# Performance work log

Hardware: AMD Instinct MI355X
Metric: run time of the kernel (lower is better)

The kernel has to match this reference:

```python
import math
import jax, jax.numpy as jnp
import numpy as np

DIM = 256
HEADS = 4
TAU = 1e-3
TOPK = 64


def setup_inputs() -> dict:
    key = jax.random.key(0)
    ks = jax.random.split(key, 11)
    B, N, D = 4, 1024, DIM
    s = 1.0 / math.sqrt(D)
    return {
        "F_cls": jax.random.normal(ks[0], (B, N, D), jnp.float32),
        "F_seg": jax.random.normal(ks[1], (B, N, D), jnp.float32),
        "F_age": jax.random.normal(ks[2], (B, N, D), jnp.float32),
        "Wq": jax.random.normal(ks[3], (D, D), jnp.float32) * s,
        "bq": jnp.zeros((D,), jnp.float32),
        "Wk": jax.random.normal(ks[4], (D, D), jnp.float32) * s,
        "bk": jnp.zeros((D,), jnp.float32),
        "Wv": jax.random.normal(ks[5], (D, D), jnp.float32) * s,
        "bv": jnp.zeros((D,), jnp.float32),
        "Wo": jax.random.normal(ks[6], (D, D), jnp.float32) * s,
        "bo": jnp.zeros((D,), jnp.float32),
    }


def reference(F_cls, F_seg, F_age, Wq, bq, Wk, bk, Wv, bv, Wo, bo):
    # Concatenate the three task branches along tokens: (B, 3N, D)
    X = jnp.concatenate([F_cls, F_seg, F_age], axis=1)
    # L1 soft-thresholding
    Xs = jnp.sign(X) * jnp.maximum(jnp.abs(X) - TAU, 0.0)
    B, TN, D = Xs.shape
    N = F_cls.shape[1]
    H, Dh = HEADS, D // HEADS
    # per-sample channel saliency and top-k channel mask
    sal = jnp.abs(Xs).mean(axis=1)                      # (B, D)
    _, idx = jax.lax.top_k(sal, TOPK)                   # (B, k)
    mask = jnp.zeros((B, D), bool).at[jnp.arange(B)[:, None], idx].set(True)
    Xt = Xs * mask[:, None, :]                          # (B, TN, D)
    # shared K/V over all tokens; Q over all tokens equals the concat of the
    # three per-branch q_proj outputs (same weights), so one fused attention
    # is mathematically identical to the three original calls.
    Q = Xt @ Wq.T + bq
    K = Xt @ Wk.T + bk
    V = Xt @ Wv.T + bv
    def heads(x):
        return x.reshape(B, TN, H, Dh).transpose(0, 2, 1, 3)  # (B,H,TN,Dh)
    Qh, Kh, Vh = heads(Q), heads(K), heads(V)
    logits = jnp.einsum("bhqd,bhkd->bhqk", Qh, Kh) / math.sqrt(Dh)
    A = jax.nn.softmax(logits, axis=-1)
    out = jnp.einsum("bhqk,bhkd->bhqd", A, Vh)
    out = out.transpose(0, 2, 1, 3).reshape(B, TN, D)
    out = out @ Wo.T + bo
    return (out[:, 0:N], out[:, N:2 * N], out[:, 2 * N:3 * N])
```

## Files before the change

### kernel.cpp

```cpp
#include <hip/hip_runtime.h>
#include <math.h>

typedef __attribute__((ext_vector_type(8))) short bf16x8;
typedef __attribute__((ext_vector_type(16))) float f32x16;

#define Bsz 4
#define Nn 1024
#define TN 3072
#define Dd 256
#define Hh 4
#define DH 64
#define TAUc 1e-3f
#define QSCALE 0.1803368801111f

#define SALP_OFF 0
#define IDX_OFF  98304
#define XCB_OFF  98560
#define WCT_OFF  491776
#define QB_OFF   590080
#define KB_OFF   2162944
#define VT_OFF   3735808
#define OP0_OFF  5308672
#define OP1_OFF  8454400
#define SML_OFF  11600128

__device__ __forceinline__ ushort f2b(float f) {
    uint u = __float_as_uint(f);
    u += 0x7fffu + ((u >> 16) & 1u);
    return (ushort)(u >> 16);
}
__device__ __forceinline__ uint pk2(float a, float b) {
    return (uint)f2b(a) | ((uint)f2b(b) << 16);
}
__device__ __forceinline__ uint trunc_pk(float a, float b) {
    return (__float_as_uint(a) >> 16) | (__float_as_uint(b) & 0xFFFF0000u);
}
__device__ __forceinline__ float hi_f(float a) {
    return __uint_as_float(__float_as_uint(a) & 0xFFFF0000u);
}
__device__ __forceinline__ uint cvtpk(float a, float b) {
    uint r;
    asm("v_cvt_pk_bf16_f32 %0, %1, %2" : "=v"(r) : "v"(a), "v"(b));
    return r;
}
__device__ __forceinline__ float ex2(float x) {
    return __builtin_amdgcn_exp2f(x);
}
__device__ __forceinline__ void gld16(const ushort* g, ushort* l) {
    __builtin_amdgcn_global_load_lds(
        (const __attribute__((address_space(1))) uint*)g,
        (__attribute__((address_space(3))) uint*)l, 16, 0, 0);
}
union U4B8 { uint u[4]; bf16x8 v; };
__device__ __forceinline__ bf16x8 ld8(const ushort* p) { return *(const bf16x8*)p; }

__global__ __launch_bounds__(256) void k_sal(
        const float* __restrict__ F0, const float* __restrict__ F1,
        const float* __restrict__ F2, float* __restrict__ salp) {
    int b = blockIdx.x / 96;
    int slab = blockIdx.x - b * 96;
    int t0 = slab * 32;
    int seg = t0 >> 10, tt0 = t0 & 1023;
    const float* F = (seg == 0) ? F0 : (seg == 1 ? F1 : F2);
    const float* base = &F[(size_t)((b << 10) + tt0) * Dd + threadIdx.x];
    float acc = 0.f;
    #pragma unroll 4
    for (int r = 0; r < 32; ++r) {
        float x = base[(size_t)r * Dd];
        acc += fmaxf(fabsf(x) - TAUc, 0.f);
    }
    salp[blockIdx.x * 256 + threadIdx.x] = acc;
}

__global__ void k_topk(const float* __restrict__ salp, int* __restrict__ idx) {
    __shared__ float v[256];
    __shared__ int cnt;
    int b = blockIdx.x, tid = threadIdx.x;
    float myval = 0.f;
    const float* p = &salp[(size_t)b * 96 * 256 + tid];
    #pragma unroll 4
    for (int s = 0; s < 96; ++s) myval += p[s * 256];
    v[tid] = myval;
    if (tid == 0) cnt = 0;
    __syncthreads();
    for (int k = 2; k <= 256; k <<= 1)
        for (int j = k >> 1; j > 0; j >>= 1) {
            int ixj = tid ^ j;
            if (ixj > tid) {
                float a = v[tid], c = v[ixj];
                bool up = ((tid & k) == 0);
                if ((a > c) == up) { v[tid] = c; v[ixj] = a; }
            }
            __syncthreads();
        }
    float thr = v[192];
    if (myval >= thr) {
        int p2 = atomicAdd(&cnt, 1);
        if (p2 < 64) idx[b * 64 + p2] = tid;
    }
}

__global__ __launch_bounds__(256) void k_gather(
        const float* __restrict__ F0, const float* __restrict__ F1,
        const float* __restrict__ F2,
        const float* __restrict__ Wq, const float* __restrict__ Wk,
        const float* __restrict__ Wv, const int* __restrict__ idx,
        uint* __restrict__ Xcb, uint* __restrict__ Wct) {
    __shared__ float xs[32 * 260];
    __shared__ int ids[64];
    int tid = threadIdx.x;
    if (blockIdx.x < 384) {
        int b = blockIdx.x / 96;
        int t0 = (blockIdx.x - b * 96) * 32;
        if (tid < 64) ids[tid] = idx[b * 64 + tid];
        int seg = t0 >> 10, tt0 = t0 & 1023;
        const float* F = (seg == 0) ? F0 : (seg == 1 ? F1 : F2);
        const float* base = &F[(size_t)((b << 10) + tt0) * Dd];
        #pragma unroll
        for (int i = 0; i < 8; ++i) {
            int i0 = tid + i * 256;
            int r = i0 >> 6, c4 = (i0 & 63) << 2;
            float4 x = *(const float4*)&base[(size_t)r * Dd + c4];
            x.x = copysignf(fmaxf(fabsf(x.x) - TAUc, 0.f), x.x);
            x.y = copysignf(fmaxf(fabsf(x.y) - TAUc, 0.f), x.y);
            x.z = copysignf(fmaxf(fabsf(x.z) - TAUc, 0.f), x.z);
            x.w = copysignf(fmaxf(fabsf(x.w) - TAUc, 0.f), x.w);
            *(float4*)&xs[r * 260 + c4] = x;
        }
        __syncthreads();
        #pragma unroll
        for (int i = 0; i < 4; ++i) {
            int i0 = tid + i * 256;
            int r = i0 >> 5, jp = i0 & 31;
            float x0 = xs[r * 260 + ids[2 * jp]];
            float x1 = xs[r * 260 + ids[2 * jp + 1]];
            Xcb[(size_t)(b * TN + t0 + r) * 32 + jp] = pk2(x0, x1);
        }
    } else {
        int gid = (blockIdx.x - 384) * 256 + tid;
        int b = gid / 24576;
        if (tid < 64) ids[tid] = idx[b * 64 + tid];
        __syncthreads();
        int rem = gid - b * 24576;
        int mat = rem / 8192;
        int rem2 = rem - mat * 8192;
        int dout = rem2 >> 5, jp = rem2 & 31;
        const float* Wm = (mat == 0) ? Wq : (mat == 1 ? Wk : Wv);
        float w0 = Wm[(size_t)dout * 256 + ids[2 * jp]];
        float w1 = Wm[(size_t)dout * 256 + ids[2 * jp + 1]];
        Wct[((size_t)(b * 3 + mat) * 256 + dout) * 32 + jp] = pk2(w0, w1);
    }
}

__global__ __launch_bounds__(256) void k_qkv(
        const ushort* __restrict__ Xcb, const ushort* __restrict__ Wct,
        const float* __restrict__ bq, const float* __restrict__ bk,
        const float* __restrict__ bv,
        ushort* __restrict__ Qh, ushort* __restrict__ Kh, ushort* __restrict__ Vt) {
    int wave = threadIdx.x >> 6, lane = threadIdx.x & 63;
    int l31 = lane & 31, h = lane >> 5;
    int W = blockIdx.x * 4 + wave;
    int b = W / 576;
    int r = W - b * 576;
    int mat = r / 192;
    int p = r - mat * 192;
    const ushort* Xb = Xcb + (size_t)b * TN * 64;
    const ushort* Wm = Wct + (size_t)(b * 3 + mat) * 256 * 64;
    f32x16 c[4];
    #pragma unroll
    for (int nt = 0; nt < 4; ++nt)
        #pragma unroll
        for (int q = 0; q < 16; ++q) c[nt][q] = 0.f;
    if (mat < 2) {
        int mtt = p % 96, ng = p / 96;
        const ushort* arow = &Xb[(size_t)(mtt * 32 + l31) * 64];
        #pragma unroll
        for (int kc = 0; kc < 4; ++kc) {
            bf16x8 af = ld8(arow + kc * 16 + 8 * h);
            #pragma unroll
            for (int nt = 0; nt < 4; ++nt) {
                bf16x8 bf = ld8(&Wm[(size_t)(ng * 128 + nt * 32 + l31) * 64 + kc * 16 + 8 * h]);
                c[nt] = __builtin_amdgcn_mfma_f32_32x32x16_bf16(af, bf, c[nt], 0, 0, 0);
            }
        }
        if (mat == 0) {
            #pragma unroll
            for (int nt = 0; nt < 4; ++nt) {
                int dout = ng * 128 + nt * 32 + l31;
                int head = dout >> 6, d63 = dout & 63;
                float bb = bq[dout];
                size_t obase = ((size_t)(b * 4 + head) * TN + mtt * 32) * 64 + d63;
                #pragma unroll
                for (int u = 0; u < 16; ++u) {
                    int trow = (u & 3) + 8 * (u >> 2) + 4 * h;
                    Qh[obase + (size_t)trow * 64] = f2b((c[nt][u] + bb) * QSCALE);
                }
            }
        } else {
            #pragma unroll
            for (int nt = 0; nt < 4; ++nt) {
                int dout = ng * 128 + nt * 32 + l31;
                int head = dout >> 6, d63 = dout & 63;
                float bb = bk[dout];
                size_t base = (size_t)(b * 4 + head) * 196608;
                #pragma unroll
                for (int u = 0; u < 16; ++u) {
                    int trow = (u & 3) + 8 * (u >> 2) + 4 * h;
                    int t = mtt * 32 + trow;
                    int row = t & 127, tile = t >> 7;
                    int fk = (row ^ (row >> 3)) & 7;
                    Kh[base + (size_t)tile * 8192 + row * 64 +
                       (((d63 >> 3) ^ fk) << 3) + (d63 & 7)] = f2b(c[nt][u] + bb);
                }
            }
        }
    } else {
        int mtv = p & 7, tg = p >> 3;
        const ushort* arow = &Wm[(size_t)(mtv * 32 + l31) * 64];
        #pragma unroll
        for (int kc = 0; kc < 4; ++kc) {
            bf16x8 af = ld8(arow + kc * 16 + 8 * h);
            #pragma unroll
            for (int nt = 0; nt < 4; ++nt) {
                bf16x8 bf = ld8(&Xb[(size_t)(tg * 128 + nt * 32 + l31) * 64 + kc * 16 + 8 * h]);
                c[nt] = __builtin_amdgcn_mfma_f32_32x32x16_bf16(af, bf, c[nt], 0, 0, 0);
            }
        }
        int head = mtv >> 1;
        int sl = (l31 & 19) | ((l31 & 4) << 1) | ((l31 & 8) >> 1);
        size_t vbase = (size_t)(b * 4 + head) * 196608 + (size_t)tg * 8192;
        #pragma unroll
        for (int nt = 0; nt < 4; ++nt) {
            int cc = (nt * 32 + sl) >> 3;
            int elem = sl & 7;
            #pragma unroll
            for (int u = 0; u < 16; ++u) {
                int dout = mtv * 32 + (u & 3) + 8 * (u >> 2) + 4 * h;
                int row = dout & 63;
                int fv = (row ^ (row >> 3)) & 7;
                int ch = (cc & 8) | ((cc & 7) ^ fv);
                Vt[vbase + row * 128 + ch * 8 + elem] = f2b(c[nt][u] + bv[dout]);
            }
        }
    }
}

__global__ __launch_bounds__(256, 3) void k_attn(
        const ushort* __restrict__ Qg, const ushort* __restrict__ Kg,
        const ushort* __restrict__ Vtg,
        float* __restrict__ OP0, float* __restrict__ OP1,
        float* __restrict__ Sml) {
    __shared__ __align__(16) ushort Ks[2][64 * 64];
    __shared__ __align__(16) ushort Vts[2][64 * 64];
    int bid = blockIdx.x;
    int xcd = bid & 7, j0 = bid >> 3;
    int bh = xcd * 2 + (j0 / 48);
    int rem = j0 % 48;
    int qt = rem >> 1, ksplit = rem & 1;
    int b = bh >> 2, hh = bh & 3;
    int tid = threadIdx.x, wave = tid >> 6, lane = tid & 63;
    int l31 = lane & 31, h = lane >> 5;
    int q0 = qt * 128 + wave * 32;
    const ushort* Qb = Qg + ((size_t)bh * TN + q0 + l31) * DH;
    bf16x8 qf[4];
    #pragma unroll
    for (int kc = 0; kc < 4; ++kc) qf[kc] = ld8(&Qb[kc * 16 + 8 * h]);

    const ushort* Ktb = Kg + (size_t)bh * 196608 + (size_t)ksplit * 98304;
    const ushort* Vtb = Vtg + (size_t)bh * 196608 + (size_t)ksplit * 98304;

    int koff0 = tid * 8, koff1 = tid * 8 + 2048;
    int voff0 = (tid >> 3) * 128 + (tid & 7) * 8;
    int voff1 = voff0 + 4096;

    f32x16 o0, o1;
    #pragma unroll
    for (int q = 0; q < 16; ++q) { o0[q] = 0.f; o1[q] = 0.f; }
    f32x16 zf;
    #pragma unroll
    for (int q = 0; q < 16; ++q) zf[q] = 0.f;
    float lrun = 0.f;

    int fq0 = (l31 ^ (l31 >> 3)) & 7;
    int fq1 = ((32 + l31) ^ ((32 + l31) >> 3)) & 7;
    int r0c = l31 * 64, r1c = (32 + l31) * 64;

    auto stage = [&](int ht, ushort* KsD, ushort* VtsD) {
        const ushort* ksrc = Ktb + (size_t)ht * 4096;
        const ushort* vsrc = Vtb + (size_t)((ht >> 1) * 8192 + (ht & 1) * 64);
        gld16(ksrc + koff0, KsD + koff0);
        gld16(ksrc + koff1, KsD + koff1);
        gld16(vsrc + voff0, VtsD + koff0);
        gld16(vsrc + voff1, VtsD + koff1);
    };

    auto compute = [&](const ushort* KsB, const ushort* VtsB) {
        f32x16 s0, s1;
        __builtin_amdgcn_s_setprio(1);
        {
            bf16x8 k0 = ld8(&KsB[r0c + ((h ^ fq0) << 3)]);
            s0 = __builtin_amdgcn_mfma_f32_32x32x16_bf16(k0, qf[0], zf, 0, 0, 0);
        }
        #pragma unroll
        for (int kc = 1; kc < 4; ++kc) {
            bf16x8 k0 = ld8(&KsB[r0c + (((2 * kc + h) ^ fq0) << 3)]);
            s0 = __builtin_amdgcn_mfma_f32_32x32x16_bf16(k0, qf[kc], s0, 0, 0, 0);
        }
        {
            bf16x8 k1 = ld8(&KsB[r1c + ((h ^ fq1) << 3)]);
            s1 = __builtin_amdgcn_mfma_f32_32x32x16_bf16(k1, qf[0], zf, 0, 0, 0);
        }
        #pragma unroll
        for (int kc = 1; kc < 4; ++kc) {
            bf16x8 k1 = ld8(&KsB[r1c + (((2 * kc + h) ^ fq1) << 3)]);
            s1 = __builtin_amdgcn_mfma_f32_32x32x16_bf16(k1, qf[kc], s1, 0, 0, 0);
        }
        __builtin_amdgcn_s_setprio(0);
        U4B8 pk4[4];
        float ps0 = 0.f, ps1 = 0.f, ps2 = 0.f, ps3 = 0.f;
        #pragma unroll
        for (int u = 0; u < 8; ++u) {
            float pa = ex2(s0[2 * u]), pb = ex2(s0[2 * u + 1]);
            ps0 += pa; ps1 += pb;
            pk4[u >> 2].u[u & 3] = cvtpk(pa, pb);
        }
        __builtin_amdgcn_s_setprio(1);
        #pragma unroll
        for (int kc2 = 0; kc2 < 2; ++kc2) {
            int ch = 2 * kc2 + h;
            bf16x8 v0f = ld8(&VtsB[r0c + ((ch ^ fq0) << 3)]);
            bf16x8 v1f = ld8(&VtsB[r1c + ((ch ^ fq1) << 3)]);
            o0 = __builtin_amdgcn_mfma_f32_32x32x16_bf16(pk4[kc2].v, v0f, o0, 0, 0, 0);
            o1 = __builtin_amdgcn_mfma_f32_32x32x16_bf16(pk4[kc2].v, v1f, o1, 0, 0, 0);
        }
        __builtin_amdgcn_s_setprio(0);
        #pragma unroll
        for (int u = 0; u < 8; ++u) {
            float pa = ex2(s1[2 * u]), pb = ex2(s1[2 * u + 1]);
            ps2 += pa; ps3 += pb;
            pk4[2 + (u >> 2)].u[u & 3] = cvtpk(pa, pb);
        }
        lrun += (ps0 + ps1) + (ps2 + ps3);
        __builtin_amdgcn_s_setprio(1);
        #pragma unroll
        for (int kc2 = 2; kc2 < 4; ++kc2) {
            int ch = 2 * kc2 + h;
            bf16x8 v0f = ld8(&VtsB[r0c + ((ch ^ fq0) << 3)]);
            bf16x8 v1f = ld8(&VtsB[r1c + ((ch ^ fq1) << 3)]);
            o0 = __builtin_amdgcn_mfma_f32_32x32x16_bf16(pk4[kc2].v, v0f, o0, 0, 0, 0);
            o1 = __builtin_amdgcn_mfma_f32_32x32x16_bf16(pk4[kc2].v, v1f, o1, 0, 0, 0);
        }
        __builtin_amdgcn_s_setprio(0);
    };

    stage(0, Ks[0], Vts[0]);
    __syncthreads();
    #pragma unroll 1
    for (int t = 0; t < 24; t += 2) {
        stage(t + 1, Ks[1], Vts[1]);
        compute(Ks[0], Vts[0]);
        __syncthreads();
        if (t + 2 < 24) stage(t + 2, Ks[0], Vts[0]);
        compute(Ks[1], Vts[1]);
        __syncthreads();
    }

    lrun += __shfl_xor(lrun, 32);

    float* OP = ksplit ? OP1 : OP0;
    #pragma unroll
    for (int q = 0; q < 16; ++q) {
        int qrow = (q & 3) + 8 * (q >> 2) + 4 * h;
        int t = q0 + qrow;
        size_t base = ((size_t)b * TN + t) * Dd + hh * 64;
        OP[base + l31] = o0[q];
        OP[base + 32 + l31] = o1[q];
    }
    if (h == 0)
        Sml[(size_t)ksplit * 49152 + (size_t)bh * TN + q0 + l31] = lrun;
}

__global__ __launch_bounds__(256) void k_out(
        const float* __restrict__ OP0, const float* __restrict__ OP1,
        const float* __restrict__ Sml, const float* __restrict__ Wo,
        const float* __restrict__ bo, float* __restrict__ out) {
    __shared__ __align__(16) ushort Ms[2][64][64];
    __shared__ float invsh[64 * 4];
    int nd4 = blockIdx.y;
    int R0 = blockIdx.x * 64;
    int b = R0 / TN;
    int tloc0 = R0 - b * TN;
    int tid = threadIdx.x, wave = tid >> 6, lane = tid & 63;
    int l31 = lane & 31, h = lane >> 5;
    int wt = wave & 1, wd = wave >> 1;
    {
        int hd = tid >> 6, t = tid & 63;
        size_t o = (size_t)(b * 4 + hd) * TN + tloc0 + t;
        invsh[t * 4 + hd] = 1.f / (Sml[o] + Sml[49152 + o]);
    }
    int dout = nd4 * 64 + wd * 32 + l31;
    float bb = bo[dout];
    const float* wrow = &Wo[(size_t)dout * 256];
    int st_t = tid >> 2, st_c = tid & 3;
    int fst = (st_t ^ (st_t >> 3)) & 7;
    size_t gbase = ((size_t)(b * TN + tloc0 + st_t)) * 256 + st_c * 8;
    int trow = wt * 32 + l31;
    int ftr = (trow ^ (trow >> 3)) & 7;
    f32x16 acc;
    #pragma unroll
    for (int q = 0; q < 16; ++q) acc[q] = 0.f;

    auto stage_load = [&](int st, int buf) {
        size_t ob = gbase + (size_t)st * 32;
        float4 x0 = *(const float4*)&OP0[ob];
        float4 x1 = *(const float4*)&OP0[ob + 4];
        float4 y0 = *(const float4*)&OP1[ob];
        float4 y1 = *(const float4*)&OP1[ob + 4];
        float s = invsh[st_t * 4 + (st >> 1)];
        float m0 = (x0.x + y0.x) * s, m1 = (x0.y + y0.y) * s;
        float m2 = (x0.z + y0.z) * s, m3 = (x0.w + y0.w) * s;
        float m4 = (x1.x + y1.x) * s, m5 = (x1.y + y1.y) * s;
        float m6 = (x1.z + y1.z) * s, m7 = (x1.w + y1.w) * s;
        uint4 hi = { trunc_pk(m0, m1), trunc_pk(m2, m3),
                     trunc_pk(m4, m5), trunc_pk(m6, m7) };
        uint4 lo = { trunc_pk(m0 - hi_f(m0), m1 - hi_f(m1)),
                     trunc_pk(m2 - hi_f(m2), m3 - hi_f(m3)),
                     trunc_pk(m4 - hi_f(m4), m5 - hi_f(m5)),
                     trunc_pk(m6 - hi_f(m6), m7 - hi_f(m7)) };
        *(uint4*)&Ms[buf][st_t][(st_c ^ fst) * 8] = hi;
        *(uint4*)&Ms[buf][st_t][((4 + st_c) ^ fst) * 8] = lo;
    };

    __syncthreads();
    stage_load(0, 0);
    #pragma unroll 1
    for (int st = 0; st < 8; ++st) {
        __syncthreads();
        if (st < 7) stage_load(st + 1, (st + 1) & 1);
        int buf = st & 1;
        #pragma unroll
        for (int kc = 0; kc < 2; ++kc) {
            bf16x8 ah = *(const bf16x8*)&Ms[buf][trow][((2 * kc + h) ^ ftr) * 8];
            bf16x8 al = *(const bf16x8*)&Ms[buf][trow][((4 + 2 * kc + h) ^ ftr) * 8];
            int din0 = st * 32 + kc * 16 + 8 * h;
            float4 w0 = *(const float4*)&wrow[din0];
            float4 w1 = *(const float4*)&wrow[din0 + 4];
            U4B8 wh, wl;
            wh.u[0] = trunc_pk(w0.x, w0.y); wh.u[1] = trunc_pk(w0.z, w0.w);
            wh.u[2] = trunc_pk(w1.x, w1.y); wh.u[3] = trunc_pk(w1.z, w1.w);
            wl.u[0] = trunc_pk(w0.x - hi_f(w0.x), w0.y - hi_f(w0.y));
            wl.u[1] = trunc_pk(w0.z - hi_f(w0.z), w0.w - hi_f(w0.w));
            wl.u[2] = trunc_pk(w1.x - hi_f(w1.x), w1.y - hi_f(w1.y));
            wl.u[3] = trunc_pk(w1.z - hi_f(w1.z), w1.w - hi_f(w1.w));
            acc = __builtin_amdgcn_mfma_f32_32x32x16_bf16(ah, wh.v, acc, 0, 0, 0);
            acc = __builtin_amdgcn_mfma_f32_32x32x16_bf16(al, wh.v, acc, 0, 0, 0);
            acc = __builtin_amdgcn_mfma_f32_32x32x16_bf16(ah, wl.v, acc, 0, 0, 0);
        }
    }
    #pragma unroll
    for (int u = 0; u < 16; ++u) {
        int tloc = tloc0 + wt * 32 + (u & 3) + 8 * (u >> 2) + 4 * h;
        int chunk = tloc >> 10, tt = tloc & 1023;
        out[(size_t)chunk * (Bsz * Nn * Dd) + ((size_t)(b * Nn + tt)) * Dd + dout] =
            acc[u] + bb;
    }
}

extern "C" void kernel_launch(void* const* d_in, const int* in_sizes, int n_in,
                              void* d_out, int out_size, void* d_ws, size_t ws_size,
                              hipStream_t stream) {
    const float* F0 = (const float*)d_in[0];
    const float* F1 = (const float*)d_in[1];
    const float* F2 = (const float*)d_in[2];
    const float* Wq = (const float*)d_in[3];
    const float* bq = (const float*)d_in[4];
    const float* Wk = (const float*)d_in[5];
    const float* bk = (const float*)d_in[6];
    const float* Wv = (const float*)d_in[7];
    const float* bv = (const float*)d_in[8];
    const float* Wo = (const float*)d_in[9];
    const float* bo = (const float*)d_in[10];
    float* ws = (float*)d_ws;
    float* out = (float*)d_out;

    int* idxp = (int*)(ws + IDX_OFF);
    uint* Xcb = (uint*)(ws + XCB_OFF);
    uint* Wct = (uint*)(ws + WCT_OFF);
    ushort* Qb16 = (ushort*)(ws + QB_OFF);
    ushort* Kb16 = (ushort*)(ws + KB_OFF);
    ushort* Vt16 = (ushort*)(ws + VT_OFF);
    float* OP0 = ws + OP0_OFF;
    float* OP1 = ws + OP1_OFF;
    float* Sml = ws + SML_OFF;

    k_sal<<<384, 256, 0, stream>>>(F0, F1, F2, ws + SALP_OFF);
    k_topk<<<Bsz, 256, 0, stream>>>(ws + SALP_OFF, idxp);
    k_gather<<<768, 256, 0, stream>>>(F0, F1, F2, Wq, Wk, Wv, idxp, Xcb, Wct);
    k_qkv<<<576, 256, 0, stream>>>((const ushort*)Xcb, (const ushort*)Wct,
                                   bq, bk, bv, Qb16, Kb16, Vt16);
    k_attn<<<768, 256, 0, stream>>>(Qb16, Kb16, Vt16, OP0, OP1, Sml);
    k_out<<<dim3(192, 4), 256, 0, stream>>>(OP0, OP1, Sml, Wo, bo, out);
}
```

Before: 171.4 us.

## Generalize attention key-split to four partitions when workspace allows

Parameterizes the flash-attention key split so k_attn can divide the key sequence into four chunks instead of two. When the workspace is large enough this doubles the grid to 1536 blocks, and k_out sums four partial outputs and denominators. Launch bounds rise to 5 blocks per SM to improve occupancy and latency hiding. The cost is more partial-output memory traffic in k_out and shorter per-block loops with more prologue overhead.

```diff
diff --git a/kernel.cpp b/kernel.cpp
--- a/kernel.cpp
+++ b/kernel.cpp
@@ -21,8 +21,10 @@
 #define KB_OFF   2162944
 #define VT_OFF   3735808
 #define OP0_OFF  5308672
-#define OP1_OFF  8454400
-#define SML_OFF  11600128
+#define OPSTR    3145728
+#define SML2_OFF 11600128
+#define SML4_OFF 17891584
+#define WS4_NEED ((size_t)(17891584 + 4 * 49152) * 4)
 
 __device__ __forceinline__ ushort f2b(float f) {
     uint u = __float_as_uint(f);
@@ -245,18 +247,21 @@
     }
 }
 
-__global__ __launch_bounds__(256, 3) void k_attn(
+__global__ __launch_bounds__(256, 5) void k_attn(
         const ushort* __restrict__ Qg, const ushort* __restrict__ Kg,
         const ushort* __restrict__ Vtg,
-        float* __restrict__ OP0, float* __restrict__ OP1,
-        float* __restrict__ Sml) {
+        float* __restrict__ OPb, float* __restrict__ Sml, int nspl) {
     __shared__ __align__(16) ushort Ks[2][64 * 64];
     __shared__ __align__(16) ushort Vts[2][64 * 64];
     int bid = blockIdx.x;
     int xcd = bid & 7, j0 = bid >> 3;
-    int bh = xcd * 2 + (j0 / 48);
-    int rem = j0 % 48;
-    int qt = rem >> 1, ksplit = rem & 1;
+    int pb = 24 * nspl;
+    int bhl = j0 / pb;
+    int bh = xcd * 2 + bhl;
+    int rem = j0 - bhl * pb;
+    int qt = rem / nspl;
+    int ks = rem - qt * nspl;
+    int nhalf = 48 / nspl;
     int b = bh >> 2, hh = bh & 3;
     int tid = threadIdx.x, wave = tid >> 6, lane = tid & 63;
     int l31 = lane & 31, h = lane >> 5;
@@ -266,8 +271,8 @@
     #pragma unroll
     for (int kc = 0; kc < 4; ++kc) qf[kc] = ld8(&Qb[kc * 16 + 8 * h]);
 
-    const ushort* Ktb = Kg + (size_t)bh * 196608 + (size_t)ksplit * 98304;
-    const ushort* Vtb = Vtg + (size_t)bh * 196608 + (size_t)ksplit * 98304;
+    const ushort* Ktb = Kg + (size_t)bh * 196608 + (size_t)ks * (nhalf * 4096);
+    const ushort* Vtb = Vtg + (size_t)bh * 196608 + (size_t)ks * (nhalf * 4096);
 
     int koff0 = tid * 8, koff1 = tid * 8 + 2048;
     int voff0 = (tid >> 3) * 128 + (tid & 7) * 8;
@@ -320,9 +325,9 @@
         float ps0 = 0.f, ps1 = 0.f, ps2 = 0.f, ps3 = 0.f;
         #pragma unroll
         for (int u = 0; u < 8; ++u) {
-            float pa = ex2(s0[2 * u]), pb = ex2(s0[2 * u + 1]);
-            ps0 += pa; ps1 += pb;
-            pk4[u >> 2].u[u & 3] = cvtpk(pa, pb);
+            float pa = ex2(s0[2 * u]), pb2 = ex2(s0[2 * u + 1]);
+            ps0 += pa; ps1 += pb2;
+            pk4[u >> 2].u[u & 3] = cvtpk(pa, pb2);
         }
         __builtin_amdgcn_s_setprio(1);
         #pragma unroll
@@ -336,9 +341,9 @@
         __builtin_amdgcn_s_setprio(0);
         #pragma unroll
         for (int u = 0; u < 8; ++u) {
-            float pa = ex2(s1[2 * u]), pb = ex2(s1[2 * u + 1]);
-            ps2 += pa; ps3 += pb;
-            pk4[2 + (u >> 2)].u[u & 3] = cvtpk(pa, pb);
+            float pa = ex2(s1[2 * u]), pb2 = ex2(s1[2 * u + 1]);
+            ps2 += pa; ps3 += pb2;
+            pk4[2 + (u >> 2)].u[u & 3] = cvtpk(pa, pb2);
         }
         lrun += (ps0 + ps1) + (ps2 + ps3);
         __builtin_amdgcn_s_setprio(1);
@@ -356,18 +361,18 @@
     stage(0, Ks[0], Vts[0]);
     __syncthreads();
     #pragma unroll 1
-    for (int t = 0; t < 24; t += 2) {
+    for (int t = 0; t < nhalf; t += 2) {
         stage(t + 1, Ks[1], Vts[1]);
         compute(Ks[0], Vts[0]);
         __syncthreads();
-        if (t + 2 < 24) stage(t + 2, Ks[0], Vts[0]);
+        if (t + 2 < nhalf) stage(t + 2, Ks[0], Vts[0]);
         compute(Ks[1], Vts[1]);
         __syncthreads();
     }
 
     lrun += __shfl_xor(lrun, 32);
 
-    float* OP = ksplit ? OP1 : OP0;
+    float* OP = OPb + (size_t)ks * OPSTR;
     #pragma unroll
     for (int q = 0; q < 16; ++q) {
         int qrow = (q & 3) + 8 * (q >> 2) + 4 * h;
@@ -377,13 +382,13 @@
         OP[base + 32 + l31] = o1[q];
     }
     if (h == 0)
-        Sml[(size_t)ksplit * 49152 + (size_t)bh * TN + q0 + l31] = lrun;
+        Sml[(size_t)ks * 49152 + (size_t)bh * TN + q0 + l31] = lrun;
 }
 
 __global__ __launch_bounds__(256) void k_out(
-        const float* __restrict__ OP0, const float* __restrict__ OP1,
-        const float* __restrict__ Sml, const float* __restrict__ Wo,
-        const float* __restrict__ bo, float* __restrict__ out) {
+        const float* __restrict__ OPb, const float* __restrict__ Sml,
+        const float* __restrict__ Wo, const float* __restrict__ bo,
+        float* __restrict__ out, int nspl) {
     __shared__ __align__(16) ushort Ms[2][64][64];
     __shared__ float invsh[64 * 4];
     int nd4 = blockIdx.y;
@@ -396,7 +401,10 @@
     {
         int hd = tid >> 6, t = tid & 63;
         size_t o = (size_t)(b * 4 + hd) * TN + tloc0 + t;
-        invsh[t * 4 + hd] = 1.f / (Sml[o] + Sml[49152 + o]);
+        float ssum = 0.f;
+        #pragma unroll 2
+        for (int sp = 0; sp < nspl; ++sp) ssum += Sml[(size_t)sp * 49152 + o];
+        invsh[t * 4 + hd] = 1.f / ssum;
     }
     int dout = nd4 * 64 + wd * 32 + l31;
     float bb = bo[dout];
@@ -412,15 +420,19 @@
 
     auto stage_load = [&](int st, int buf) {
         size_t ob = gbase + (size_t)st * 32;
-        float4 x0 = *(const float4*)&OP0[ob];
-        float4 x1 = *(const float4*)&OP0[ob + 4];
-        float4 y0 = *(const float4*)&OP1[ob];
-        float4 y1 = *(const float4*)&OP1[ob + 4];
+        float a0 = 0.f, a1 = 0.f, a2 = 0.f, a3 = 0.f;
+        float a4 = 0.f, a5 = 0.f, a6 = 0.f, a7 = 0.f;
+        #pragma unroll 2
+        for (int sp = 0; sp < nspl; ++sp) {
+            const float* P = OPb + (size_t)sp * OPSTR;
+            float4 u0 = *(const float4*)&P[ob];
+            float4 u1 = *(const float4*)&P[ob + 4];
+            a0 += u0.x; a1 += u0.y; a2 += u0.z; a3 += u0.w;
+            a4 += u1.x; a5 += u1.y; a6 += u1.z; a7 += u1.w;
+        }
         float s = invsh[st_t * 4 + (st >> 1)];
-        float m0 = (x0.x + y0.x) * s, m1 = (x0.y + y0.y) * s;
-        float m2 = (x0.z + y0.z) * s, m3 = (x0.w + y0.w) * s;
-        float m4 = (x1.x + y1.x) * s, m5 = (x1.y + y1.y) * s;
-        float m6 = (x1.z + y1.z) * s, m7 = (x1.w + y1.w) * s;
+        float m0 = a0 * s, m1 = a1 * s, m2 = a2 * s, m3 = a3 * s;
+        float m4 = a4 * s, m5 = a5 * s, m6 = a6 * s, m7 = a7 * s;
         uint4 hi = { trunc_pk(m0, m1), trunc_pk(m2, m3),
                      trunc_pk(m4, m5), trunc_pk(m6, m7) };
         uint4 lo = { trunc_pk(m0 - hi_f(m0), m1 - hi_f(m1)),
@@ -490,14 +502,15 @@
     ushort* Kb16 = (ushort*)(ws + KB_OFF);
     ushort* Vt16 = (ushort*)(ws + VT_OFF);
     float* OP0 = ws + OP0_OFF;
-    float* OP1 = ws + OP1_OFF;
-    float* Sml = ws + SML_OFF;
+
+    int nspl = (ws_size >= WS4_NEED) ? 4 : 2;
+    float* Sml = (nspl == 4) ? (ws + SML4_OFF) : (ws + SML2_OFF);
 
     k_sal<<<384, 256, 0, stream>>>(F0, F1, F2, ws + SALP_OFF);
     k_topk<<<Bsz, 256, 0, stream>>>(ws + SALP_OFF, idxp);
     k_gather<<<768, 256, 0, stream>>>(F0, F1, F2, Wq, Wk, Wv, idxp, Xcb, Wct);
     k_qkv<<<576, 256, 0, stream>>>((const ushort*)Xcb, (const ushort*)Wct,
                                    bq, bk, bv, Qb16, Kb16, Vt16);
-    k_attn<<<768, 256, 0, stream>>>(Qb16, Kb16, Vt16, OP0, OP1, Sml);
-    k_out<<<dim3(192, 4), 256, 0, stream>>>(OP0, OP1, Sml, Wo, bo, out);
-}
+    k_attn<<<384 * nspl, 256, 0, stream>>>(Qb16, Kb16, Vt16, OP0, Sml, nspl);
+    k_out<<<dim3(192, 4), 256, 0, stream>>>(OP0, Sml, Wo, bo, out, nspl);
+}
```

Result: slower. 438.9 us (+156.0%).

## Pre-split Wo into bf16 hi/lo once and use shuffle-based bitonic top-k

Applied to the files above, without the earlier changes.

Adds 64 extra blocks to the gather kernel that convert Wo once into packed bf16 hi and lo halves in workspace. k_out then loads those ready-made operands instead of re-splitting fp32 weights in every block and k-step, which halves the weight bytes read and removes the per-step conversion ALU work. Separately, the top-k bitonic sort keeps values in registers and uses wave shuffles for strides below 64, so it only goes through shared memory and barriers for the larger strides. Costs are a little more workspace and a slightly longer gather launch.

```diff
diff --git a/kernel.cpp b/kernel.cpp
--- a/kernel.cpp
+++ b/kernel.cpp
@@ -23,6 +23,7 @@
 #define OP0_OFF  5308672
 #define OP1_OFF  8454400
 #define SML_OFF  11600128
+#define WOP_OFF  11698432
 
 __device__ __forceinline__ ushort f2b(float f) {
     uint u = __float_as_uint(f);
@@ -73,27 +74,35 @@
 }
 
 __global__ void k_topk(const float* __restrict__ salp, int* __restrict__ idx) {
-    __shared__ float v[256];
+    __shared__ float xw[256];
+    __shared__ float thrs;
     __shared__ int cnt;
     int b = blockIdx.x, tid = threadIdx.x;
     float myval = 0.f;
     const float* p = &salp[(size_t)b * 96 * 256 + tid];
     #pragma unroll 4
     for (int s = 0; s < 96; ++s) myval += p[s * 256];
-    v[tid] = myval;
     if (tid == 0) cnt = 0;
+    float v = myval;
+    for (int k = 2; k <= 256; k <<= 1) {
+        for (int j = k >> 1; j > 0; j >>= 1) {
+            bool up = ((tid & k) == 0);
+            float ov;
+            if (j >= 64) {
+                xw[tid] = v;
+                __syncthreads();
+                ov = xw[tid ^ j];
+                __syncthreads();
+            } else {
+                ov = __shfl_xor(v, j);
+            }
+            bool lowhalf = ((tid & j) == 0);
+            v = (lowhalf == up) ? fminf(v, ov) : fmaxf(v, ov);
+        }
+    }
+    if (tid == 192) thrs = v;
     __syncthreads();
-    for (int k = 2; k <= 256; k <<= 1)
-        for (int j = k >> 1; j > 0; j >>= 1) {
-            int ixj = tid ^ j;
-            if (ixj > tid) {
-                float a = v[tid], c = v[ixj];
-                bool up = ((tid & k) == 0);
-                if ((a > c) == up) { v[tid] = c; v[ixj] = a; }
-            }
-            __syncthreads();
-        }
-    float thr = v[192];
+    float thr = thrs;
     if (myval >= thr) {
         int p2 = atomicAdd(&cnt, 1);
         if (p2 < 64) idx[b * 64 + p2] = tid;
@@ -104,8 +113,10 @@
         const float* __restrict__ F0, const float* __restrict__ F1,
         const float* __restrict__ F2,
         const float* __restrict__ Wq, const float* __restrict__ Wk,
-        const float* __restrict__ Wv, const int* __restrict__ idx,
-        uint* __restrict__ Xcb, uint* __restrict__ Wct) {
+        const float* __restrict__ Wv, const float* __restrict__ Wo,
+        const int* __restrict__ idx,
+        uint* __restrict__ Xcb, uint* __restrict__ Wct,
+        uint* __restrict__ Wop) {
     __shared__ float xs[32 * 260];
     __shared__ int ids[64];
     int tid = threadIdx.x;
@@ -136,7 +147,7 @@
             float x1 = xs[r * 260 + ids[2 * jp + 1]];
             Xcb[(size_t)(b * TN + t0 + r) * 32 + jp] = pk2(x0, x1);
         }
-    } else {
+    } else if (blockIdx.x < 768) {
         int gid = (blockIdx.x - 384) * 256 + tid;
         int b = gid / 24576;
         if (tid < 64) ids[tid] = idx[b * 64 + tid];
@@ -149,6 +160,15 @@
         float w0 = Wm[(size_t)dout * 256 + ids[2 * jp]];
         float w1 = Wm[(size_t)dout * 256 + ids[2 * jp + 1]];
         Wct[((size_t)(b * 3 + mat) * 256 + dout) * 32 + jp] = pk2(w0, w1);
+    } else {
+        int gid2 = (blockIdx.x - 768) * 256 + tid;
+        int dout = gid2 >> 6, g = gid2 & 63;
+        float4 w = *(const float4*)&Wo[(size_t)dout * 256 + g * 4];
+        uint* row = &Wop[(size_t)dout * 256];
+        row[g * 2]       = trunc_pk(w.x, w.y);
+        row[g * 2 + 1]   = trunc_pk(w.z, w.w);
+        row[128 + g * 2] = trunc_pk(w.x - hi_f(w.x), w.y - hi_f(w.y));
+        row[128 + g * 2 + 1] = trunc_pk(w.z - hi_f(w.z), w.w - hi_f(w.w));
     }
 }
 
@@ -382,7 +402,7 @@
 
 __global__ __launch_bounds__(256) void k_out(
         const float* __restrict__ OP0, const float* __restrict__ OP1,
-        const float* __restrict__ Sml, const float* __restrict__ Wo,
+        const float* __restrict__ Sml, const uint* __restrict__ Wop,
         const float* __restrict__ bo, float* __restrict__ out) {
     __shared__ __align__(16) ushort Ms[2][64][64];
     __shared__ float invsh[64 * 4];
@@ -400,7 +420,7 @@
     }
     int dout = nd4 * 64 + wd * 32 + l31;
     float bb = bo[dout];
-    const float* wrow = &Wo[(size_t)dout * 256];
+    const uint* wrow = &Wop[(size_t)dout * 256];
     int st_t = tid >> 2, st_c = tid & 3;
     int fst = (st_t ^ (st_t >> 3)) & 7;
     size_t gbase = ((size_t)(b * TN + tloc0 + st_t)) * 256 + st_c * 8;
@@ -443,18 +463,11 @@
             bf16x8 ah = *(const bf16x8*)&Ms[buf][trow][((2 * kc + h) ^ ftr) * 8];
             bf16x8 al = *(const bf16x8*)&Ms[buf][trow][((4 + 2 * kc + h) ^ ftr) * 8];
             int din0 = st * 32 + kc * 16 + 8 * h;
-            float4 w0 = *(const float4*)&wrow[din0];
-            float4 w1 = *(const float4*)&wrow[din0 + 4];
-            U4B8 wh, wl;
-            wh.u[0] = trunc_pk(w0.x, w0.y); wh.u[1] = trunc_pk(w0.z, w0.w);
-            wh.u[2] = trunc_pk(w1.x, w1.y); wh.u[3] = trunc_pk(w1.z, w1.w);
-            wl.u[0] = trunc_pk(w0.x - hi_f(w0.x), w0.y - hi_f(w0.y));
-            wl.u[1] = trunc_pk(w0.z - hi_f(w0.z), w0.w - hi_f(w0.w));
-            wl.u[2] = trunc_pk(w1.x - hi_f(w1.x), w1.y - hi_f(w1.y));
-            wl.u[3] = trunc_pk(w1.z - hi_f(w1.z), w1.w - hi_f(w1.w));
-            acc = __builtin_amdgcn_mfma_f32_32x32x16_bf16(ah, wh.v, acc, 0, 0, 0);
-            acc = __builtin_amdgcn_mfma_f32_32x32x16_bf16(al, wh.v, acc, 0, 0, 0);
-            acc = __builtin_amdgcn_mfma_f32_32x32x16_bf16(ah, wl.v, acc, 0, 0, 0);
+            bf16x8 whv = *(const bf16x8*)&wrow[din0 >> 1];
+            bf16x8 wlv = *(const bf16x8*)&wrow[128 + (din0 >> 1)];
+            acc = __builtin_amdgcn_mfma_f32_32x32x16_bf16(ah, whv, acc, 0, 0, 0);
+            acc = __builtin_amdgcn_mfma_f32_32x32x16_bf16(al, whv, acc, 0, 0, 0);
+            acc = __builtin_amdgcn_mfma_f32_32x32x16_bf16(ah, wlv, acc, 0, 0, 0);
         }
     }
     #pragma unroll
@@ -492,12 +505,14 @@
     float* OP0 = ws + OP0_OFF;
     float* OP1 = ws + OP1_OFF;
     float* Sml = ws + SML_OFF;
+    uint* Wop = (uint*)(ws + WOP_OFF);
 
     k_sal<<<384, 256, 0, stream>>>(F0, F1, F2, ws + SALP_OFF);
     k_topk<<<Bsz, 256, 0, stream>>>(ws + SALP_OFF, idxp);
-    k_gather<<<768, 256, 0, stream>>>(F0, F1, F2, Wq, Wk, Wv, idxp, Xcb, Wct);
+    k_gather<<<832, 256, 0, stream>>>(F0, F1, F2, Wq, Wk, Wv, Wo, idxp,
+                                      Xcb, Wct, Wop);
     k_qkv<<<576, 256, 0, stream>>>((const ushort*)Xcb, (const ushort*)Wct,
                                    bq, bk, bv, Qb16, Kb16, Vt16);
     k_attn<<<768, 256, 0, stream>>>(Qb16, Kb16, Vt16, OP0, OP1, Sml);
-    k_out<<<dim3(192, 4), 256, 0, stream>>>(OP0, OP1, Sml, Wo, bo, out);
-}
+    k_out<<<dim3(192, 4), 256, 0, stream>>>(OP0, OP1, Sml, Wop, bo, out);
+}
```

Result: no change. 170.8 us (-0.3%).
